# Kernel tuning notes

Hardware: AMD Instinct MI355X
Metric: run time of the kernel (lower is better)

## Reference

```python
import jax, jax.numpy as jnp
import numpy as np

B, C, HF, WF = 2, 128, 60, 80
N = 3072
T = 16.0          # min(t_base + epoch, t_max), saturated
WIN_HALF = 0.125  # config['window_size'] (normalized half-width)
WIN_STEPS = 9     # window sampling grid side
EPS = 1e-6

def l2norm(x, axis):
    return x / jnp.sqrt(jnp.sum(x * x, axis=axis, keepdims=True) + 1e-12)

def denorm(cn, h, w):
    # normalized [-1,1] (x,y) -> pixel coords
    return (cn + 1.0) * 0.5 * jnp.array([w - 1.0, h - 1.0], cn.dtype)

def norm_coords(c, h, w):
    return c * (2.0 / jnp.array([w - 1.0, h - 1.0], c.dtype)) - 1.0

def bilinear_sample(fmap, cn):
    """fmap (b,C,H,W); cn (b,M,2) normalized (x,y); align_corners=True, border pad."""
    b, Cc, H, W = fmap.shape
    x = (cn[..., 0] + 1.0) * 0.5 * (W - 1)
    y = (cn[..., 1] + 1.0) * 0.5 * (H - 1)
    x0 = jnp.floor(x); y0 = jnp.floor(y)
    wx = x - x0; wy = y - y0
    x0i = jnp.clip(x0.astype(jnp.int32), 0, W - 1)
    x1i = jnp.clip(x0i + 1, 0, W - 1)
    y0i = jnp.clip(y0.astype(jnp.int32), 0, H - 1)
    y1i = jnp.clip(y0i + 1, 0, H - 1)
    gb = jax.vmap(lambda fm, yi, xi: fm[:, yi, xi])  # (C,M) per batch
    f00 = gb(fmap, y0i, x0i); f01 = gb(fmap, y0i, x1i)
    f10 = gb(fmap, y1i, x0i); f11 = gb(fmap, y1i, x1i)
    wx = wx[:, None, :]; wy = wy[:, None, :]
    out = f00 * (1 - wx) * (1 - wy) + f01 * wx * (1 - wy) + f10 * (1 - wx) * wy + f11 * wx * wy
    return jnp.transpose(out, (0, 2, 1))  # (b,M,C)

def window_search(feat1, fmap2_t, center_n):
    """Expected correspondence within a window. feat1 (b,N,C); fmap2_t pre-scaled by T."""
    b, n, Cc = feat1.shape
    lin = jnp.linspace(-WIN_HALF, WIN_HALF, WIN_STEPS).astype(feat1.dtype)
    gy, gx = jnp.meshgrid(lin, lin, indexing='ij')
    offs = jnp.stack([gx.ravel(), gy.ravel()], -1)         # (S,2)
    S = offs.shape[0]
    wc = center_n[:, :, None, :] + offs[None, None]         # (b,N,S,2)
    feats = bilinear_sample(fmap2_t, wc.reshape(b, n * S, 2)).reshape(b, n, S, Cc)
    prob = jax.nn.softmax(jnp.einsum('bnc,bnsc->bns', feat1, feats), axis=-1)
    exp_n = jnp.einsum('bns,bnsd->bnd', prob, wc)
    var = jnp.einsum('bns,bnsd->bnd', prob, wc ** 2) - exp_n ** 2
    std = jnp.sqrt(jnp.clip(var, EPS)).sum(-1)
    return exp_n, wc, std

def setup_inputs() -> dict:
    key = jax.random.key(0)
    k1, k2, k3, k4 = jax.random.split(key, 4)
    xf1 = jax.random.normal(k1, (B, C, HF, WF), jnp.float32)
    xf2 = jax.random.normal(k2, (B, C, HF, WF), jnp.float32)
    coord1_n = jax.random.uniform(k3, (B, N, 2), jnp.float32) * 2.0 - 1.0
    coord2_n = jax.random.uniform(k4, (B, N, 2), jnp.float32) * 2.0 - 1.0
    return {"xf1": xf1, "xf2": xf2, "coord1_n": coord1_n, "coord2_n": coord2_n,
            "h1i": 480, "w1i": 640, "h2i": 480, "w2i": 640}

def reference(xf1, xf2, coord1_n, coord2_n, h1i, w1i, h2i, w2i):
    coord1 = denorm(coord1_n, h1i, w1i)
    coord2 = denorm(coord2_n, h2i, w2i)
    f1 = l2norm(bilinear_sample(xf1, coord1_n), -1)  # cos distance -> L2-normalized
    f2 = l2norm(bilinear_sample(xf2, coord2_n), -1)
    cos_sim = jnp.einsum('bnc,bmc->bnm', f1, f2)      # (b,N,N)
    p12 = jax.nn.softmax(T * cos_sim, axis=2)
    p21 = jax.nn.softmax(T * cos_sim, axis=1)
    g1 = jnp.einsum('bnm,bmd->bnd', p12, coord2)      # feat1g_corloc
    g2 = jnp.einsum('bnm,bnd->bmd', p21, coord1)      # feat2g_corloc
    g1n = jax.lax.stop_gradient(norm_coords(g1, h2i, w2i))
    g2n = jax.lax.stop_gradient(norm_coords(g2, h1i, w1i))
    std1 = jnp.sqrt(jnp.clip(jnp.einsum('bnm,bmd->bnd', p12, coord2_n ** 2) - g1n ** 2, EPS)).sum(-1)
    std2 = jnp.sqrt(jnp.clip(jnp.einsum('bnm,bnd->bmd', p21, coord1_n ** 2) - g2n ** 2, EPS)).sum(-1)
    # use_line_search=False branch: window centers are the detached global corloc
    xf2t = T * l2norm(xf2, 1)
    xf1t = T * l2norm(xf1, 1)
    w1n, _, wstd1 = window_search(f1, xf2t, g1n)
    w2n, _, wstd2 = window_search(f2, xf1t, g2n)
    w1 = denorm(w1n, h2i, w2i)  # feat1w_corloc
    w2 = denorm(w2n, h1i, w1i)  # feat2w_corloc
    valid1 = jnp.ones(std1.shape, dtype=bool)
    valid2 = jnp.ones(std2.shape, dtype=bool)
    return (coord1, coord2, g1, g2, w1, w2, g1n, g2n, std1, std2, wstd1, wstd2, valid1, valid2)
```

## Files before the change

kernel.cpp:

```cpp
#include <hip/hip_runtime.h>
#include <hip/hip_bf16.h>
#include <math.h>

#define BB 2
#define CC 128
#define HH 60
#define WW 80
#define NN 3072
#define TT 16.0f
#define SS 81
#define HW (HH*WW)
#define NTILE 24
#define LDA 136
#define XN 12
#define YN 10

typedef __attribute__((ext_vector_type(8))) short short8;
typedef __attribute__((ext_vector_type(4))) float f32x4;
typedef _Float16 hf;
typedef _Float16 __attribute__((ext_vector_type(2))) h2;

#if __has_builtin(__builtin_amdgcn_fdot2)
#define FDOT2(a,b,c) __builtin_amdgcn_fdot2((a),(b),(c),false)
#else
#define FDOT2(a,b,c) ((c) + (float)(a).x*(float)(b).x + (float)(a).y*(float)(b).y)
#endif

template<int CTRL>
__device__ __forceinline__ float dppterm(float s){
    return __int_as_float(__builtin_amdgcn_update_dpp(0, __float_as_int(s), CTRL, 0xf, 0xf, true));
}
__device__ __forceinline__ float red8_add(float s){
    s += dppterm<0xB1>(s); s += dppterm<0x4E>(s); s += dppterm<0x141>(s); return s;
}
__device__ __forceinline__ float red16_add(float s){
    s += dppterm<0xB1>(s); s += dppterm<0x4E>(s); s += dppterm<0x141>(s); s += dppterm<0x140>(s); return s;
}
__device__ __forceinline__ float swz16_add(float s){
    return s + __int_as_float(__builtin_amdgcn_ds_swizzle(__float_as_int(s), 0x401F));
}
__device__ __forceinline__ float red64_add(float s){
    s = red16_add(s); s = swz16_add(s); s += __shfl_xor(s, 32); return s;
}
__device__ __forceinline__ float red64_max(float s){
    s = fmaxf(s, dppterm<0xB1>(s)); s = fmaxf(s, dppterm<0x4E>(s));
    s = fmaxf(s, dppterm<0x141>(s)); s = fmaxf(s, dppterm<0x140>(s));
    s = fmaxf(s, __int_as_float(__builtin_amdgcn_ds_swizzle(__float_as_int(s), 0x401F)));
    s = fmaxf(s, __shfl_xor(s, 32));
    return s;
}

__device__ __forceinline__ void bsetup(float cn, int L, int& i0, int& i1, float& w){
    float x = (cn + 1.0f) * 0.5f * (float)(L - 1);
    float x0 = floorf(x);
    w = x - x0;
    int xi = (int)x0;
    i0 = xi < 0 ? 0 : (xi > L - 1 ? L - 1 : xi);
    i1 = (i0 + 1 > L - 1) ? L - 1 : (i0 + 1);
}

__global__ __launch_bounds__(256) void k_normT(
        const float* __restrict__ xf1, const float* __restrict__ xf2,
        hf* __restrict__ xf1r, hf* __restrict__ xf2r,
        hf* __restrict__ xf1t, hf* __restrict__ xf2t){
    int idx = blockIdx.x;
    int map = idx / (BB*(HW/32));
    int rem = idx % (BB*(HW/32));
    int b   = rem / (HW/32);
    int hw0 = (rem % (HW/32)) * 32;
    const float* src = (map ? xf2 : xf1) + (size_t)b*CC*HW + hw0;
    hf* dstR = (map ? xf2r : xf1r) + ((size_t)(b*HW + hw0))*CC;
    hf* dstT = (map ? xf2t : xf1t) + ((size_t)(b*HW + hw0))*CC;

    __shared__ float tile[CC][33];
    int tid = threadIdx.x;
    {
        int p = tid & 31, c0 = tid >> 5;
        #pragma unroll
        for(int i=0;i<16;i++){
            int c = i*8 + c0;
            tile[c][p] = src[(size_t)c*HW + p];
        }
    }
    __syncthreads();
    int q = tid >> 3, l = tid & 7;
    float v[16];
    float ss = 0.f;
    #pragma unroll
    for(int k=0;k<16;k++){ v[k] = tile[l*16+k][q]; ss += v[k]*v[k]; }
    ss = red8_add(ss);
    float inv = 1.0f / sqrtf(ss + 1e-12f);
    float tsc = TT * inv;
    union { hf h[16]; uint4 u[2]; } R, T;
    #pragma unroll
    for(int k=0;k<16;k++){ R.h[k] = (hf)v[k]; T.h[k] = (hf)(v[k]*tsc); }
    uint4* oR = (uint4*)(dstR + (size_t)q*CC + l*16);
    uint4* oT = (uint4*)(dstT + (size_t)q*CC + l*16);
    oR[0] = R.u[0]; oR[1] = R.u[1];
    oT[0] = T.u[0]; oT[1] = T.u[1];
}

__global__ __launch_bounds__(256) void k_feats(
        const hf* __restrict__ xf1r, const hf* __restrict__ xf2r,
        const float* __restrict__ c1n, const float* __restrict__ c2n,
        __hip_bfloat16* __restrict__ f1b, __hip_bfloat16* __restrict__ f2b,
        float* __restrict__ o_coord1, float* __restrict__ o_coord2,
        const int* __restrict__ h1I, const int* __restrict__ w1I,
        const int* __restrict__ h2I, const int* __restrict__ w2I){
    int tid = threadIdx.x;
    int gid = blockIdx.x*4 + (tid >> 6);
    int dir = gid / (BB*NN);
    int bn  = gid % (BB*NN);
    int b = bn / NN;
    const hf* raw = dir ? xf2r : xf1r;
    const float* cn = dir ? c2n : c1n;
    __hip_bfloat16* fOutB = dir ? f2b : f1b;
    float* coordOut = dir ? o_coord2 : o_coord1;
    const int* hI = dir ? h2I : h1I;
    const int* wI = dir ? w2I : w1I;

    int t = tid & 63;
    float cnx = cn[(size_t)bn*2+0], cny = cn[(size_t)bn*2+1];
    int x0,x1,y0,y1; float wx,wy;
    bsetup(cnx, WW, x0,x1,wx);
    bsetup(cny, HH, y0,y1,wy);
    const hf* base = raw + (size_t)(b*HW)*CC;
    const uint* r00 = (const uint*)(base + (size_t)(y0*WW+x0)*CC) + t;
    const uint* r01 = (const uint*)(base + (size_t)(y0*WW+x1)*CC) + t;
    const uint* r10 = (const uint*)(base + (size_t)(y1*WW+x0)*CC) + t;
    const uint* r11 = (const uint*)(base + (size_t)(y1*WW+x1)*CC) + t;
    union { uint u; h2 v; } u00, u01, u10, u11;
    u00.u = *r00; u01.u = *r01; u10.u = *r10; u11.u = *r11;
    float w00=(1.f-wx)*(1.f-wy), w01=wx*(1.f-wy), w10=(1.f-wx)*wy, w11=wx*wy;
    float fx = w00*(float)u00.v.x + w01*(float)u01.v.x + w10*(float)u10.v.x + w11*(float)u11.v.x;
    float fy = w00*(float)u00.v.y + w01*(float)u01.v.y + w10*(float)u10.v.y + w11*(float)u11.v.y;
    float ss = fx*fx + fy*fy;
    ss = red64_add(ss);
    float inv = 1.0f / sqrtf(ss + 1e-12f);
    unsigned short blo = __bfloat16_as_ushort(__float2bfloat16(fx*inv));
    unsigned short bhi = __bfloat16_as_ushort(__float2bfloat16(fy*inv));
    ((uint*)(fOutB + (size_t)bn*CC))[t] = ((uint)bhi << 16) | blo;
    if(t==0){
        float h=(float)hI[0], w=(float)wI[0];
        coordOut[(size_t)bn*2+0] = (cnx+1.0f)*0.5f*(w-1.0f);
        coordOut[(size_t)bn*2+1] = (cny+1.0f)*0.5f*(h-1.0f);
    }
}

__global__ __launch_bounds__(512,4) void k_corr(
        const __hip_bfloat16* __restrict__ f1b, const __hip_bfloat16* __restrict__ f2b,
        const float* __restrict__ c1n, const float* __restrict__ c2n,
        float* __restrict__ wsRow, float* __restrict__ wsCol,
        const int* __restrict__ h1I, const int* __restrict__ w1I,
        const int* __restrict__ h2I, const int* __restrict__ w2I){
    const int nwg = BB*NTILE*NTILE;
    int blk = blockIdx.x;
    blk = (blk & 7)*(nwg/8) + (blk >> 3);
    int b   = blk / (NTILE*NTILE);
    int rem = blk % (NTILE*NTILE);
    int nt = rem / NTILE, mt = rem % NTILE;
    int n0 = nt*128, m0 = mt*128;
    int tid = threadIdx.x;
    int lane = tid & 63, wid = tid >> 6;
    int wr = wid >> 1, wc = wid & 1;
    int lr = lane & 15, lh = lane >> 4;

    __shared__ __align__(16) unsigned short As[128*LDA];
    __shared__ __align__(16) unsigned short Bs[128*LDA];
    float* partsF = (float*)As;
    const int COLOFF = 2*128*8;

    {
        const unsigned short* gA = (const unsigned short*)f1b + ((size_t)b*NN + n0)*CC;
        const unsigned short* gB = (const unsigned short*)f2b + ((size_t)b*NN + m0)*CC;
        #pragma unroll
        for(int it=0; it<4; ++it){
            int idx = tid + it*512;
            int r = idx >> 4, q = idx & 15;
            *(uint4*)(As + r*LDA + q*8) = *(const uint4*)(gA + r*CC + q*8);
            *(uint4*)(Bs + r*LDA + q*8) = *(const uint4*)(gB + r*CC + q*8);
        }
    }

    float2 c2v[4], c1v[8];
    #pragma unroll
    for(int j=0;j<4;j++)
        c2v[j] = ((const float2*)c2n)[(size_t)b*NN + m0 + wc*64 + j*16 + lr];
    #pragma unroll
    for(int i=0;i<2;i++)
        #pragma unroll
        for(int r=0;r<4;r++)
            c1v[i*4+r] = ((const float2*)c1n)[(size_t)b*NN + n0 + wr*32 + i*16 + lh*4 + r];

    __syncthreads();

    f32x4 acc[2][4] = {};
    const unsigned short* aBase = As + (wr*32 + lr)*LDA + lh*8;
    const unsigned short* bBase = Bs + (wc*64 + lr)*LDA + lh*8;
    #pragma unroll
    for(int ks=0; ks<4; ++ks){
        short8 afr[2], bfr[4];
        #pragma unroll
        for(int i=0;i<2;i++) afr[i] = *(const short8*)(aBase + i*16*LDA + ks*32);
        #pragma unroll
        for(int j=0;j<4;j++) bfr[j] = *(const short8*)(bBase + j*16*LDA + ks*32);
        #pragma unroll
        for(int i=0;i<2;i++)
            #pragma unroll
            for(int j=0;j<4;j++)
                acc[i][j] = __builtin_amdgcn_mfma_f32_16x16x32_bf16(afr[i], bfr[j], acc[i][j], 0,0,0);
    }
    __syncthreads();

    const float TL2E = 23.08312035f;
    float h1f=(float)h1I[0], w1f=(float)w1I[0], h2f=(float)h2I[0], w2f=(float)w2I[0];
    float sx2 = 0.5f*(w2f-1.0f), sy2 = 0.5f*(h2f-1.0f);
    float sx1 = 0.5f*(w1f-1.0f), sy1 = 0.5f*(h1f-1.0f);

    float cx2[4], cy2[4], cxx2[4], cyy2[4];
    #pragma unroll
    for(int j=0;j<4;j++){
        cx2[j] = (c2v[j].x+1.f)*sx2; cy2[j] = (c2v[j].y+1.f)*sy2;
        cxx2[j] = c2v[j].x*c2v[j].x; cyy2[j] = c2v[j].y*c2v[j].y;
    }
    float colA[4][5] = {};
    #pragma unroll
    for(int i=0;i<2;i++){
        #pragma unroll
        for(int r=0;r<4;r++){
            float2 c1 = c1v[i*4+r];
            float cx1=(c1.x+1.f)*sx1, cy1=(c1.y+1.f)*sy1;
            float cxx1=c1.x*c1.x, cyy1=c1.y*c1.y;
            float rs=0.f, rax=0.f, ray=0.f, raxx=0.f, rayy=0.f;
            #pragma unroll
            for(int j=0;j<4;j++){
                float wgt = exp2f(fmaf(TL2E, acc[i][j][r], -TL2E));
                rs += wgt;
                rax  = fmaf(wgt, cx2[j],  rax);
                ray  = fmaf(wgt, cy2[j],  ray);
                raxx = fmaf(wgt, cxx2[j], raxx);
                rayy = fmaf(wgt, cyy2[j], rayy);
                colA[j][0] += wgt;
                colA[j][1] = fmaf(wgt, cx1,  colA[j][1]);
                colA[j][2] = fmaf(wgt, cy1,  colA[j][2]);
                colA[j][3] = fmaf(wgt, cxx1, colA[j][3]);
                colA[j][4] = fmaf(wgt, cyy1, colA[j][4]);
            }
            rs   = red16_add(rs);
            rax  = red16_add(rax);
            ray  = red16_add(ray);
            raxx = red16_add(raxx);
            rayy = red16_add(rayy);
            if(lr==0){
                int nl = wr*32 + i*16 + lh*4 + r;
                float* rp = partsF + ((size_t)wc*128 + nl)*8;
                *(float4*)rp = make_float4(rs, rax, ray, raxx);
                rp[4] = rayy;
            }
        }
    }
    #pragma unroll
    for(int j=0;j<4;j++){
        #pragma unroll
        for(int c=0;c<5;c++){
            colA[j][c] = swz16_add(colA[j][c]);
            colA[j][c] += __shfl_xor(colA[j][c], 32);
        }
        if(lh==0){
            int ml = wc*64 + j*16 + lr;
            float* cp = partsF + COLOFF + ((size_t)wr*128 + ml)*8;
            *(float4*)cp = make_float4(colA[j][0], colA[j][1], colA[j][2], colA[j][3]);
            cp[4] = colA[j][4];
        }
    }
    __syncthreads();

    if(tid < 128){
        int p = tid;
        size_t basep = (size_t)b*NN + n0 + p;
        float4 r0 = *(float4*)(partsF + ((size_t)0*128 + p)*8);
        float  e0 = partsF[((size_t)0*128 + p)*8 + 4];
        float4 r1 = *(float4*)(partsF + ((size_t)1*128 + p)*8);
        float  e1 = partsF[((size_t)1*128 + p)*8 + 4];
        wsRow[(size_t)(mt*5+0)*(BB*NN) + basep] = r0.x + r1.x;
        wsRow[(size_t)(mt*5+1)*(BB*NN) + basep] = r0.y + r1.y;
        wsRow[(size_t)(mt*5+2)*(BB*NN) + basep] = r0.z + r1.z;
        wsRow[(size_t)(mt*5+3)*(BB*NN) + basep] = r0.w + r1.w;
        wsRow[(size_t)(mt*5+4)*(BB*NN) + basep] = e0 + e1;
    } else if(tid < 256){
        int p = tid - 128;
        size_t basep = (size_t)b*NN + m0 + p;
        float4 s4 = make_float4(0.f,0.f,0.f,0.f);
        float  se = 0.f;
        #pragma unroll
        for(int v=0; v<4; ++v){
            float4 c4 = *(float4*)(partsF + COLOFF + ((size_t)v*128 + p)*8);
            se += partsF[COLOFF + ((size_t)v*128 + p)*8 + 4];
            s4.x += c4.x; s4.y += c4.y; s4.z += c4.z; s4.w += c4.w;
        }
        wsCol[(size_t)(nt*5+0)*(BB*NN) + basep] = s4.x;
        wsCol[(size_t)(nt*5+1)*(BB*NN) + basep] = s4.y;
        wsCol[(size_t)(nt*5+2)*(BB*NN) + basep] = s4.z;
        wsCol[(size_t)(nt*5+3)*(BB*NN) + basep] = s4.w;
        wsCol[(size_t)(nt*5+4)*(BB*NN) + basep] = se;
    }
}

__global__ __launch_bounds__(256) void k_red(
        const float* __restrict__ wsRow, const float* __restrict__ wsCol,
        float* __restrict__ o_g1, float* __restrict__ o_g1n, float* __restrict__ o_std1,
        float* __restrict__ o_g2, float* __restrict__ o_g2n, float* __restrict__ o_std2,
        float* __restrict__ o_valid,
        const int* __restrict__ h1I, const int* __restrict__ w1I,
        const int* __restrict__ h2I, const int* __restrict__ w2I){
    int p = blockIdx.x*256 + threadIdx.x;
    if(p >= 2*BB*NN) return;
    o_valid[p] = 1.0f;
    int dir = p / (BB*NN);
    int i   = p % (BB*NN);
    const float* src = (dir ? wsCol : wsRow) + i;
    float S=0.f, AX=0.f, AY=0.f, AXX=0.f, AYY=0.f;
    for(int t=0;t<NTILE;t++){
        const float* q = src + (size_t)(t*5)*(BB*NN);
        S   += q[0*(size_t)(BB*NN)];
        AX  += q[1*(size_t)(BB*NN)];
        AY  += q[2*(size_t)(BB*NN)];
        AXX += q[3*(size_t)(BB*NN)];
        AYY += q[4*(size_t)(BB*NN)];
    }
    float hf_ = dir ? (float)h1I[0] : (float)h2I[0];
    float wf = dir ? (float)w1I[0] : (float)w2I[0];
    float gx = AX/S, gy = AY/S;
    float gnx = gx * (2.0f/(wf-1.0f)) - 1.0f;
    float gny = gy * (2.0f/(hf_-1.0f)) - 1.0f;
    float vx = AXX/S - gnx*gnx;
    float vy = AYY/S - gny*gny;
    float sd = sqrtf(fmaxf(vx,1e-6f)) + sqrtf(fmaxf(vy,1e-6f));
    float* oG  = dir ? o_g2  : o_g1;
    float* oGn = dir ? o_g2n : o_g1n;
    float* oSd = dir ? o_std2: o_std1;
    oG[(size_t)i*2+0]=gx;  oG[(size_t)i*2+1]=gy;
    oGn[(size_t)i*2+0]=gnx; oGn[(size_t)i*2+1]=gny;
    oSd[i]=sd;
}

__global__ __launch_bounds__(256) void k_win2(
        const __hip_bfloat16* __restrict__ f1b, const __hip_bfloat16* __restrict__ f2b,
        const hf* __restrict__ xf1t, const hf* __restrict__ xf2t,
        const float* __restrict__ g1n, const float* __restrict__ g2n,
        float* __restrict__ o_w1, float* __restrict__ o_wstd1,
        float* __restrict__ o_w2, float* __restrict__ o_wstd2,
        const int* __restrict__ h1I, const int* __restrict__ w1I,
        const int* __restrict__ h2I, const int* __restrict__ w2I){
    int gid = blockIdx.x;
    int dir = gid / (BB*NN);
    int bn  = gid % (BB*NN);
    int b   = bn / NN;
    const __hip_bfloat16* fQ = dir ? f2b : f1b;
    const hf* fmapT          = dir ? xf1t : xf2t;
    const float* center      = dir ? g2n  : g1n;
    const int* hI            = dir ? h1I  : h2I;
    const int* wI            = dir ? w1I  : w2I;
    float* outW              = dir ? o_w2 : o_w1;
    float* outStd            = dir ? o_wstd2 : o_wstd1;

    int tid = threadIdx.x;
    int lane = tid & 63, wid = tid >> 6;
    int cg  = lane & 7;
    int sub = lane >> 3;

    float gx = center[(size_t)bn*2+0], gy = center[(size_t)bn*2+1];
    int xb, yb;
    {   int t1; float tw;
        bsetup(gx - 0.125f, WW, xb, t1, tw);
        bsetup(gy - 0.125f, HH, yb, t1, tw);
    }

    h2 fq2[8];
    {
        const uint* q = (const uint*)(fQ + (size_t)bn*CC) + cg*8;
        #pragma unroll
        for(int d=0; d<8; ++d){
            uint u = q[d];
            float lo = __uint_as_float(u << 16);
            float hi = __uint_as_float(u & 0xffff0000u);
            fq2[d].x = (hf)lo; fq2[d].y = (hf)hi;
        }
    }

    __shared__ float dl[XN*YN];
    const hf* base = fmapT + (size_t)b*HW*CC;
    #pragma unroll
    for(int it=0; it<4; ++it){
        int p = wid*30 + it*8 + sub;
        bool act = (it < 3) || (sub < 6);
        int pc = act ? p : (wid*30 + 29);
        int ky = pc / XN, kx = pc - ky*XN;
        int py = yb + ky; if(py > HH-1) py = HH-1;
        int px = xb + kx; if(px > WW-1) px = WW-1;
        const uint4* row = (const uint4*)(base + (size_t)(py*WW + px)*CC) + cg*2;
        union { uint4 u[2]; h2 v[8]; } U;
        U.u[0] = row[0]; U.u[1] = row[1];
        float s = 0.f;
        #pragma unroll
        for(int d=0; d<8; ++d) s = FDOT2(fq2[d], U.v[d], s);
        s = red8_add(s);
        if(cg==0 && act) dl[p] = s;
    }
    __syncthreads();

    float logit = -INFINITY, wcx = 0.f, wcy = 0.f;
    if(tid < SS){
        int i = tid % 9, j = tid / 9;
        wcx = gx + (-0.125f + 0.03125f*(float)i);
        wcy = gy + (-0.125f + 0.03125f*(float)j);
        int x0,x1,y0,y1; float wx,wy;
        bsetup(wcx, WW, x0,x1,wx);
        bsetup(wcy, HH, y0,y1,wy);
        int r0 = (y0-yb)*XN - xb, r1 = (y1-yb)*XN - xb;
        float d00=dl[r0+x0], d01=dl[r0+x1], d10=dl[r1+x0], d11=dl[r1+x1];
        logit = d00*(1.f-wx)*(1.f-wy) + d01*wx*(1.f-wy) + d10*(1.f-wx)*wy + d11*wx*wy;
    }

    float M = red64_max(logit);
    __shared__ float mred[4];
    if(lane==0) mred[wid] = M;
    __syncthreads();
    M = fmaxf(fmaxf(mred[0],mred[1]), fmaxf(mred[2],mred[3]));

    float w = (tid < SS) ? __expf(logit - M) : 0.f;
    float v0 = red64_add(w);
    float v1 = red64_add(w*wcx);
    float v2 = red64_add(w*wcy);
    float v3 = red64_add(w*wcx*wcx);
    float v4 = red64_add(w*wcy*wcy);
    __shared__ float sred[4][5];
    if(lane==0){ sred[wid][0]=v0; sred[wid][1]=v1; sred[wid][2]=v2; sred[wid][3]=v3; sred[wid][4]=v4; }
    __syncthreads();
    if(tid==0){
        float S  = sred[0][0]+sred[1][0]+sred[2][0]+sred[3][0];
        float ex = (sred[0][1]+sred[1][1]+sred[2][1]+sred[3][1])/S;
        float ey = (sred[0][2]+sred[1][2]+sred[2][2]+sred[3][2])/S;
        float vx = (sred[0][3]+sred[1][3]+sred[2][3]+sred[3][3])/S - ex*ex;
        float vy = (sred[0][4]+sred[1][4]+sred[2][4]+sred[3][4])/S - ey*ey;
        float sd = sqrtf(fmaxf(vx,1e-6f)) + sqrtf(fmaxf(vy,1e-6f));
        float h = (float)hI[0], wimg = (float)wI[0];
        outW[(size_t)bn*2+0] = (ex+1.0f)*0.5f*(wimg-1.0f);
        outW[(size_t)bn*2+1] = (ey+1.0f)*0.5f*(h-1.0f);
        outStd[bn] = sd;
    }
}

extern "C" void kernel_launch(void* const* d_in, const int* in_sizes, int n_in,
                              void* d_out, int out_size, void* d_ws, size_t ws_size,
                              hipStream_t stream){
    const float* xf1 = (const float*)d_in[0];
    const float* xf2 = (const float*)d_in[1];
    const float* c1n = (const float*)d_in[2];
    const float* c2n = (const float*)d_in[3];
    const int* h1 = (const int*)d_in[4];
    const int* w1 = (const int*)d_in[5];
    const int* h2 = (const int*)d_in[6];
    const int* w2 = (const int*)d_in[7];
    float* out = (float*)d_out;

    hf* xf1r = (hf*)d_ws;
    hf* xf2r = xf1r + (size_t)BB*HW*CC;
    hf* xf1t = xf2r + (size_t)BB*HW*CC;
    hf* xf2t = xf1t + (size_t)BB*HW*CC;
    __hip_bfloat16* f1b = (__hip_bfloat16*)(xf2t + (size_t)BB*HW*CC);
    __hip_bfloat16* f2b = f1b + (size_t)BB*NN*CC;
    float* wsRow = (float*)(f2b + (size_t)BB*NN*CC);
    float* wsCol = wsRow + (size_t)NTILE*5*BB*NN;

    float* o_coord1 = out + 0;
    float* o_coord2 = out + 12288;
    float* o_g1     = out + 24576;
    float* o_g2     = out + 36864;
    float* o_w1     = out + 49152;
    float* o_w2     = out + 61440;
    float* o_g1n    = out + 73728;
    float* o_g2n    = out + 86016;
    float* o_std1   = out + 98304;
    float* o_std2   = out + 104448;
    float* o_wstd1  = out + 110592;
    float* o_wstd2  = out + 116736;
    float* o_valid  = out + 122880;

    hipLaunchKernelGGL(k_normT, dim3(2*BB*(HW/32)), dim3(256), 0, stream,
                       xf1, xf2, xf1r, xf2r, xf1t, xf2t);
    hipLaunchKernelGGL(k_feats, dim3(2*BB*NN/4), dim3(256), 0, stream,
                       xf1r, xf2r, c1n, c2n, f1b, f2b, o_coord1, o_coord2, h1, w1, h2, w2);
    hipLaunchKernelGGL(k_corr, dim3(BB*NTILE*NTILE), dim3(512), 0, stream,
                       f1b, f2b, c1n, c2n, wsRow, wsCol, h1, w1, h2, w2);
    hipLaunchKernelGGL(k_red, dim3((2*BB*NN+255)/256), dim3(256), 0, stream,
                       wsRow, wsCol, o_g1, o_g1n, o_std1, o_g2, o_g2n, o_std2, o_valid,
                       h1, w1, h2, w2);
    hipLaunchKernelGGL(k_win2, dim3(2*BB*NN), dim3(256), 0, stream,
                       f1b, f2b, xf1t, xf2t, o_g1n, o_g2n,
                       o_w1, o_wstd1, o_w2, o_wstd2, h1, w1, h2, w2);
}
```

Before: 69.81 us.

## Fuse tile-partial reduction into window kernel and drop column shuffle reductions

New measurement: 69.72 us. About the same (-0.1%).

```diff
diff --git a/kernel.cpp b/kernel.cpp
--- a/kernel.cpp
+++ b/kernel.cpp
@@ -14,6 +14,7 @@
 #define LDA 136
 #define XN 12
 #define YN 10
+#define PSTRIDE 128
 
 typedef __attribute__((ext_vector_type(8))) short short8;
 typedef __attribute__((ext_vector_type(4))) float f32x4;
@@ -150,7 +151,7 @@
 __global__ __launch_bounds__(512,4) void k_corr(
         const __hip_bfloat16* __restrict__ f1b, const __hip_bfloat16* __restrict__ f2b,
         const float* __restrict__ c1n, const float* __restrict__ c2n,
-        float* __restrict__ wsRow, float* __restrict__ wsCol,
+        float* __restrict__ wsP,
         const int* __restrict__ h1I, const int* __restrict__ w1I,
         const int* __restrict__ h2I, const int* __restrict__ w2I){
     const int nwg = BB*NTILE*NTILE;
@@ -165,9 +166,10 @@
     int wr = wid >> 1, wc = wid & 1;
     int lr = lane & 15, lh = lane >> 4;
 
-    __shared__ __align__(16) unsigned short As[128*LDA];
-    __shared__ __align__(16) unsigned short Bs[128*LDA];
-    float* partsF = (float*)As;
+    __shared__ __align__(16) unsigned short smem[2*128*LDA];
+    unsigned short* As = smem;
+    unsigned short* Bs = smem + 128*LDA;
+    float* parts = (float*)smem;
     const int COLOFF = 2*128*8;
 
     {
@@ -253,7 +255,7 @@
             rayy = red16_add(rayy);
             if(lr==0){
                 int nl = wr*32 + i*16 + lh*4 + r;
-                float* rp = partsF + ((size_t)wc*128 + nl)*8;
+                float* rp = parts + ((size_t)wc*128 + nl)*8;
                 *(float4*)rp = make_float4(rs, rax, ray, raxx);
                 rp[4] = rayy;
             }
@@ -261,95 +263,54 @@
     }
     #pragma unroll
     for(int j=0;j<4;j++){
-        #pragma unroll
-        for(int c=0;c<5;c++){
-            colA[j][c] = swz16_add(colA[j][c]);
-            colA[j][c] += __shfl_xor(colA[j][c], 32);
-        }
-        if(lh==0){
-            int ml = wc*64 + j*16 + lr;
-            float* cp = partsF + COLOFF + ((size_t)wr*128 + ml)*8;
-            *(float4*)cp = make_float4(colA[j][0], colA[j][1], colA[j][2], colA[j][3]);
-            cp[4] = colA[j][4];
-        }
+        int ml = j*16 + lr;
+        float* cp = parts + COLOFF + (((size_t)wid*4 + lh)*64 + ml)*6;
+        *(float2*)cp     = make_float2(colA[j][0], colA[j][1]);
+        *(float2*)(cp+2) = make_float2(colA[j][2], colA[j][3]);
+        cp[4] = colA[j][4];
     }
     __syncthreads();
 
     if(tid < 128){
         int p = tid;
-        size_t basep = (size_t)b*NN + n0 + p;
-        float4 r0 = *(float4*)(partsF + ((size_t)0*128 + p)*8);
-        float  e0 = partsF[((size_t)0*128 + p)*8 + 4];
-        float4 r1 = *(float4*)(partsF + ((size_t)1*128 + p)*8);
-        float  e1 = partsF[((size_t)1*128 + p)*8 + 4];
-        wsRow[(size_t)(mt*5+0)*(BB*NN) + basep] = r0.x + r1.x;
-        wsRow[(size_t)(mt*5+1)*(BB*NN) + basep] = r0.y + r1.y;
-        wsRow[(size_t)(mt*5+2)*(BB*NN) + basep] = r0.z + r1.z;
-        wsRow[(size_t)(mt*5+3)*(BB*NN) + basep] = r0.w + r1.w;
-        wsRow[(size_t)(mt*5+4)*(BB*NN) + basep] = e0 + e1;
+        float4 r0 = *(float4*)(parts + ((size_t)0*128 + p)*8);
+        float  e0 = parts[((size_t)0*128 + p)*8 + 4];
+        float4 r1 = *(float4*)(parts + ((size_t)1*128 + p)*8);
+        float  e1 = parts[((size_t)1*128 + p)*8 + 4];
+        float* o = wsP + ((size_t)b*NN + n0 + p)*PSTRIDE + mt*5;
+        o[0] = r0.x + r1.x;
+        o[1] = r0.y + r1.y;
+        o[2] = r0.z + r1.z;
+        o[3] = r0.w + r1.w;
+        o[4] = e0 + e1;
     } else if(tid < 256){
         int p = tid - 128;
-        size_t basep = (size_t)b*NN + m0 + p;
-        float4 s4 = make_float4(0.f,0.f,0.f,0.f);
-        float  se = 0.f;
-        #pragma unroll
-        for(int v=0; v<4; ++v){
-            float4 c4 = *(float4*)(partsF + COLOFF + ((size_t)v*128 + p)*8);
-            se += partsF[COLOFF + ((size_t)v*128 + p)*8 + 4];
-            s4.x += c4.x; s4.y += c4.y; s4.z += c4.z; s4.w += c4.w;
-        }
-        wsCol[(size_t)(nt*5+0)*(BB*NN) + basep] = s4.x;
-        wsCol[(size_t)(nt*5+1)*(BB*NN) + basep] = s4.y;
-        wsCol[(size_t)(nt*5+2)*(BB*NN) + basep] = s4.z;
-        wsCol[(size_t)(nt*5+3)*(BB*NN) + basep] = s4.w;
-        wsCol[(size_t)(nt*5+4)*(BB*NN) + basep] = se;
-    }
-}
-
-__global__ __launch_bounds__(256) void k_red(
-        const float* __restrict__ wsRow, const float* __restrict__ wsCol,
-        float* __restrict__ o_g1, float* __restrict__ o_g1n, float* __restrict__ o_std1,
-        float* __restrict__ o_g2, float* __restrict__ o_g2n, float* __restrict__ o_std2,
-        float* __restrict__ o_valid,
-        const int* __restrict__ h1I, const int* __restrict__ w1I,
-        const int* __restrict__ h2I, const int* __restrict__ w2I){
-    int p = blockIdx.x*256 + threadIdx.x;
-    if(p >= 2*BB*NN) return;
-    o_valid[p] = 1.0f;
-    int dir = p / (BB*NN);
-    int i   = p % (BB*NN);
-    const float* src = (dir ? wsCol : wsRow) + i;
-    float S=0.f, AX=0.f, AY=0.f, AXX=0.f, AYY=0.f;
-    for(int t=0;t<NTILE;t++){
-        const float* q = src + (size_t)(t*5)*(BB*NN);
-        S   += q[0*(size_t)(BB*NN)];
-        AX  += q[1*(size_t)(BB*NN)];
-        AY  += q[2*(size_t)(BB*NN)];
-        AXX += q[3*(size_t)(BB*NN)];
-        AYY += q[4*(size_t)(BB*NN)];
-    }
-    float hf_ = dir ? (float)h1I[0] : (float)h2I[0];
-    float wf = dir ? (float)w1I[0] : (float)w2I[0];
-    float gx = AX/S, gy = AY/S;
-    float gnx = gx * (2.0f/(wf-1.0f)) - 1.0f;
-    float gny = gy * (2.0f/(hf_-1.0f)) - 1.0f;
-    float vx = AXX/S - gnx*gnx;
-    float vy = AYY/S - gny*gny;
-    float sd = sqrtf(fmaxf(vx,1e-6f)) + sqrtf(fmaxf(vy,1e-6f));
-    float* oG  = dir ? o_g2  : o_g1;
-    float* oGn = dir ? o_g2n : o_g1n;
-    float* oSd = dir ? o_std2: o_std1;
-    oG[(size_t)i*2+0]=gx;  oG[(size_t)i*2+1]=gy;
-    oGn[(size_t)i*2+0]=gnx; oGn[(size_t)i*2+1]=gny;
-    oSd[i]=sd;
+        int wcsel = p >> 6, pp = p & 63;
+        float s0=0.f,s1=0.f,s2=0.f,s3=0.f,s4=0.f;
+        #pragma unroll
+        for(int wrv=0; wrv<4; ++wrv){
+            #pragma unroll
+            for(int lh2=0; lh2<4; ++lh2){
+                const float* cp = parts + COLOFF + (((size_t)(wrv*2+wcsel)*4 + lh2)*64 + pp)*6;
+                float2 a = *(const float2*)cp;
+                float2 q = *(const float2*)(cp+2);
+                s0 += a.x; s1 += a.y; s2 += q.x; s3 += q.y; s4 += cp[4];
+            }
+        }
+        float* o = wsP + ((size_t)(BB*NN) + (size_t)b*NN + m0 + p)*PSTRIDE + nt*5;
+        o[0]=s0; o[1]=s1; o[2]=s2; o[3]=s3; o[4]=s4;
+    }
 }
 
 __global__ __launch_bounds__(256) void k_win2(
         const __hip_bfloat16* __restrict__ f1b, const __hip_bfloat16* __restrict__ f2b,
         const hf* __restrict__ xf1t, const hf* __restrict__ xf2t,
-        const float* __restrict__ g1n, const float* __restrict__ g2n,
+        const float* __restrict__ wsP,
+        float* __restrict__ o_g1, float* __restrict__ o_g1n, float* __restrict__ o_std1,
+        float* __restrict__ o_g2, float* __restrict__ o_g2n, float* __restrict__ o_std2,
         float* __restrict__ o_w1, float* __restrict__ o_wstd1,
         float* __restrict__ o_w2, float* __restrict__ o_wstd2,
+        float* __restrict__ o_valid,
         const int* __restrict__ h1I, const int* __restrict__ w1I,
         const int* __restrict__ h2I, const int* __restrict__ w2I){
     int gid = blockIdx.x;
@@ -358,18 +319,50 @@
     int b   = bn / NN;
     const __hip_bfloat16* fQ = dir ? f2b : f1b;
     const hf* fmapT          = dir ? xf1t : xf2t;
-    const float* center      = dir ? g2n  : g1n;
     const int* hI            = dir ? h1I  : h2I;
     const int* wI            = dir ? w1I  : w2I;
     float* outW              = dir ? o_w2 : o_w1;
     float* outStd            = dir ? o_wstd2 : o_wstd1;
+    float* oG                = dir ? o_g2  : o_g1;
+    float* oGn               = dir ? o_g2n : o_g1n;
+    float* oSd               = dir ? o_std2: o_std1;
 
     int tid = threadIdx.x;
     int lane = tid & 63, wid = tid >> 6;
     int cg  = lane & 7;
     int sub = lane >> 3;
 
-    float gx = center[(size_t)bn*2+0], gy = center[(size_t)bn*2+1];
+    __shared__ float acc5[5][25];
+    {
+        const float* base = wsP + ((size_t)dir*(BB*NN) + bn)*PSTRIDE;
+        if(tid < NTILE*5){
+            int mtc = tid/5, c = tid - mtc*5;
+            acc5[c][mtc] = base[tid];
+        }
+    }
+    __syncthreads();
+    if(tid < 5){
+        float s = 0.f;
+        #pragma unroll
+        for(int m=0;m<NTILE;m++) s += acc5[tid][m];
+        acc5[tid][24] = s;
+    }
+    __syncthreads();
+    float S = acc5[0][24], AX = acc5[1][24], AY = acc5[2][24];
+    float AXX = acc5[3][24], AYY = acc5[4][24];
+    float hfv = (float)hI[0], wfv = (float)wI[0];
+    float gdx = AX/S, gdy = AY/S;
+    float gx = gdx*(2.0f/(wfv-1.0f)) - 1.0f;
+    float gy = gdy*(2.0f/(hfv-1.0f)) - 1.0f;
+    if(tid == 0){
+        float vx0 = AXX/S - gx*gx, vy0 = AYY/S - gy*gy;
+        float sd0 = sqrtf(fmaxf(vx0,1e-6f)) + sqrtf(fmaxf(vy0,1e-6f));
+        oG[(size_t)bn*2+0]=gdx; oG[(size_t)bn*2+1]=gdy;
+        oGn[(size_t)bn*2+0]=gx; oGn[(size_t)bn*2+1]=gy;
+        oSd[bn]=sd0;
+        o_valid[gid]=1.0f;
+    }
+
     int xb, yb;
     {   int t1; float tw;
         bsetup(gx - 0.125f, WW, xb, t1, tw);
@@ -438,15 +431,14 @@
     if(lane==0){ sred[wid][0]=v0; sred[wid][1]=v1; sred[wid][2]=v2; sred[wid][3]=v3; sred[wid][4]=v4; }
     __syncthreads();
     if(tid==0){
-        float S  = sred[0][0]+sred[1][0]+sred[2][0]+sred[3][0];
-        float ex = (sred[0][1]+sred[1][1]+sred[2][1]+sred[3][1])/S;
-        float ey = (sred[0][2]+sred[1][2]+sred[2][2]+sred[3][2])/S;
-        float vx = (sred[0][3]+sred[1][3]+sred[2][3]+sred[3][3])/S - ex*ex;
-        float vy = (sred[0][4]+sred[1][4]+sred[2][4]+sred[3][4])/S - ey*ey;
+        float Sw = sred[0][0]+sred[1][0]+sred[2][0]+sred[3][0];
+        float ex = (sred[0][1]+sred[1][1]+sred[2][1]+sred[3][1])/Sw;
+        float ey = (sred[0][2]+sred[1][2]+sred[2][2]+sred[3][2])/Sw;
+        float vx = (sred[0][3]+sred[1][3]+sred[2][3]+sred[3][3])/Sw - ex*ex;
+        float vy = (sred[0][4]+sred[1][4]+sred[2][4]+sred[3][4])/Sw - ey*ey;
         float sd = sqrtf(fmaxf(vx,1e-6f)) + sqrtf(fmaxf(vy,1e-6f));
-        float h = (float)hI[0], wimg = (float)wI[0];
-        outW[(size_t)bn*2+0] = (ex+1.0f)*0.5f*(wimg-1.0f);
-        outW[(size_t)bn*2+1] = (ey+1.0f)*0.5f*(h-1.0f);
+        outW[(size_t)bn*2+0] = (ex+1.0f)*0.5f*(wfv-1.0f);
+        outW[(size_t)bn*2+1] = (ey+1.0f)*0.5f*(hfv-1.0f);
         outStd[bn] = sd;
     }
 }
@@ -470,8 +462,7 @@
     hf* xf2t = xf1t + (size_t)BB*HW*CC;
     __hip_bfloat16* f1b = (__hip_bfloat16*)(xf2t + (size_t)BB*HW*CC);
     __hip_bfloat16* f2b = f1b + (size_t)BB*NN*CC;
-    float* wsRow = (float*)(f2b + (size_t)BB*NN*CC);
-    float* wsCol = wsRow + (size_t)NTILE*5*BB*NN;
+    float* wsP = (float*)(f2b + (size_t)BB*NN*CC);
 
     float* o_coord1 = out + 0;
     float* o_coord2 = out + 12288;
@@ -492,11 +483,9 @@
     hipLaunchKernelGGL(k_feats, dim3(2*BB*NN/4), dim3(256), 0, stream,
                        xf1r, xf2r, c1n, c2n, f1b, f2b, o_coord1, o_coord2, h1, w1, h2, w2);
     hipLaunchKernelGGL(k_corr, dim3(BB*NTILE*NTILE), dim3(512), 0, stream,
-                       f1b, f2b, c1n, c2n, wsRow, wsCol, h1, w1, h2, w2);
-    hipLaunchKernelGGL(k_red, dim3((2*BB*NN+255)/256), dim3(256), 0, stream,
-                       wsRow, wsCol, o_g1, o_g1n, o_std1, o_g2, o_g2n, o_std2, o_valid,
-                       h1, w1, h2, w2);
+                       f1b, f2b, c1n, c2n, wsP, h1, w1, h2, w2);
     hipLaunchKernelGGL(k_win2, dim3(2*BB*NN), dim3(256), 0, stream,
-                       f1b, f2b, xf1t, xf2t, o_g1n, o_g2n,
-                       o_w1, o_wstd1, o_w2, o_wstd2, h1, w1, h2, w2);
-}
+                       f1b, f2b, xf1t, xf2t, wsP,
+                       o_g1, o_g1n, o_std1, o_g2, o_g2n, o_std2,
+                       o_w1, o_wstd1, o_w2, o_wstd2, o_valid, h1, w1, h2, w2);
+}
```
